# Kernel tuning notes

Hardware: AMD Instinct MI355X
Metric: run time of the kernel (lower is better)

Reference implementation:

```python
import jax, jax.numpy as jnp
import numpy as np

NUM_HEADS = 12

def setup_inputs() -> dict:
    key = jax.random.key(0)
    ks = jax.random.split(key, 8)
    B, N, C = 8, 1024, 768
    s = 1.0 / np.sqrt(C)
    return {
        "x": jax.random.normal(ks[0], (B, N, C), jnp.float32),
        "head_mask": jnp.ones((B, NUM_HEADS), jnp.float32),
        "q_w": jax.random.normal(ks[1], (C, C), jnp.float32) * s,
        "q_b": jnp.zeros((C,), jnp.float32),
        "k_w": jax.random.normal(ks[2], (C, C), jnp.float32) * s,
        "k_b": jnp.zeros((C,), jnp.float32),
        "v_w": jax.random.normal(ks[3], (C, C), jnp.float32) * s,
        "v_b": jnp.zeros((C,), jnp.float32),
        "proj_w": jax.random.normal(ks[4], (C, C), jnp.float32) * s,
        "proj_b": jnp.zeros((C,), jnp.float32),
    }

def reference(x, head_mask, q_w, q_b, k_w, k_b, v_w, v_b, proj_w, proj_b):
    B, N, C = x.shape
    H = NUM_HEADS
    d = C // H
    scale = d ** -0.5
    # torch Linear: y = x @ W.T + b; reshape to [B,H,N,d]
    q = (x @ q_w.T + q_b).reshape(B, N, H, d).transpose(0, 2, 1, 3)
    k = (x @ k_w.T + k_b).reshape(B, N, H, d).transpose(0, 2, 1, 3)
    v = (x @ v_w.T + v_b).reshape(B, N, H, d).transpose(0, 2, 1, 3)
    attn = jnp.einsum('bhnd,bhmd->bhnm', q, k) * scale
    attn = jax.nn.softmax(attn, axis=-1)
    y = jnp.einsum('bhnm,bhmd->bhnd', attn, v)
    # head_mask applied per head [B,H,1,1]
    y = y * head_mask[:, :, None, None]
    out = y.transpose(0, 2, 1, 3).reshape(B, N, C)
    # head_mask repeated per head_dim, applied to flattened channels [B,1,C]
    hm_flat = jnp.repeat(head_mask, d, axis=1)[:, None, :]
    out = out * hm_flat
    return out @ proj_w.T + proj_b
```

## Files before the change

kernel.cpp:

```cpp
#include <hip/hip_runtime.h>

typedef _Float16 half_t;
typedef _Float16 half2_t __attribute__((ext_vector_type(2)));
typedef _Float16 half4_t __attribute__((ext_vector_type(4)));
typedef _Float16 half8 __attribute__((ext_vector_type(8)));
typedef float f32x4 __attribute__((ext_vector_type(4)));
typedef float f32x16 __attribute__((ext_vector_type(16)));
typedef unsigned uint4v __attribute__((ext_vector_type(4)));

__device__ __forceinline__ void gload_lds16(const void* g, void* l) {
    __builtin_amdgcn_global_load_lds(
        (const __attribute__((address_space(1))) void*)g,
        (__attribute__((address_space(3))) void*)l, 16, 0, 0);
}

__global__ __launch_bounds__(256) void cast_f32_f16(const float* __restrict__ s,
                                                    half_t* __restrict__ d, int n) {
    const int stride = gridDim.x * blockDim.x;
    for (int i = blockIdx.x * blockDim.x + threadIdx.x; i * 4 < n; i += stride) {
        const float4 v = *(const float4*)(s + (long)i * 4);
        half4_t h = {(half_t)v.x, (half_t)v.y, (half_t)v.z, (half_t)v.w};
        *(half4_t*)(d + (long)i * 4) = h;
    }
}

__global__ __launch_bounds__(256) void cast_w4(const float* __restrict__ w0,
                                               const float* __restrict__ w1,
                                               const float* __restrict__ w2,
                                               const float* __restrict__ w3,
                                               half_t* __restrict__ d) {
    const int i = blockIdx.x * blockDim.x + threadIdx.x;
    const int which = i / 147456;
    const int off = i - which * 147456;
    const float* s = which == 0 ? w0 : which == 1 ? w1 : which == 2 ? w2 : w3;
    const float4 v = *(const float4*)(s + (long)off * 4);
    half4_t h = {(half_t)v.x, (half_t)v.y, (half_t)v.z, (half_t)v.w};
    *(half4_t*)(d + (long)i * 4) = h;
}

__global__ __launch_bounds__(256) void concat_bias(const float* __restrict__ a,
                                                   const float* __restrict__ b,
                                                   const float* __restrict__ c,
                                                   float* __restrict__ o) {
    int i = blockIdx.x * blockDim.x + threadIdx.x;
    if (i < 768) o[i] = a[i];
    else if (i < 1536) o[i] = b[i - 768];
    else if (i < 2304) o[i] = c[i - 1536];
}

__global__ __launch_bounds__(512) void gemm_qkv(const half_t* __restrict__ A,
                                                const half_t* __restrict__ W,
                                                const float* __restrict__ bias,
                                                half_t* __restrict__ qkv,
                                                half_t* __restrict__ Vt) {
    constexpr int Kdim = 768, Ndim = 2304, NT = Kdim / 64;
    alignas(16) __shared__ half_t Ah[2][256 * 64];
    alignas(16) __shared__ half_t Wh[2][192 * 64];

    const int t = threadIdx.x, l = t & 63, wv = t >> 6;
    const int wr = wv >> 2, wc = wv & 3;
    const int m0 = blockIdx.x * 256, n0 = blockIdx.y * 192;

    f32x4 acc[8][3] = {};

    const int srow_g = wv * 8 + (l >> 3);
    const int schunk = l & 7;

    const half_t* Ag = A + (long)m0 * Kdim;
    const half_t* Wg = W + (long)n0 * Kdim;

    auto STAGE = [&](int tile, int buf) {
        const int k0 = tile * 64;
#pragma unroll
        for (int ra = 0; ra < 4; ++ra) {
            const int row = ra * 64 + srow_g;
            const int sc_ = (schunk ^ (row & 7)) * 8;
            gload_lds16(Ag + (long)row * Kdim + k0 + sc_,
                        &Ah[buf][(ra * 64 + wv * 8) * 64]);
        }
#pragma unroll
        for (int rw = 0; rw < 3; ++rw) {
            const int row = rw * 64 + srow_g;
            const int sc_ = (schunk ^ (row & 7)) * 8;
            gload_lds16(Wg + (long)row * Kdim + k0 + sc_,
                        &Wh[buf][(rw * 64 + wv * 8) * 64]);
        }
    };

    STAGE(0, 0);
    STAGE(1, 1);

    for (int tt = 0; tt < NT; ++tt) {
        const int buf = tt & 1;
        if (tt < NT - 1) {
            asm volatile("s_waitcnt vmcnt(7)" ::: "memory");
        } else {
            asm volatile("s_waitcnt vmcnt(0)" ::: "memory");
        }
        __builtin_amdgcn_s_barrier();
        asm volatile("" ::: "memory");

#pragma unroll
        for (int ks = 0; ks < 2; ++ks) {
            const int kc = ks * 4 + (l >> 4);
            half8 bfr[3], afr[8];
#pragma unroll
            for (int nf = 0; nf < 3; ++nf) {
                const int row = wc * 48 + nf * 16 + (l & 15);
                bfr[nf] = *(const half8*)&Wh[buf][row * 64 + (kc ^ (row & 7)) * 8];
            }
#pragma unroll
            for (int mf = 0; mf < 8; ++mf) {
                const int row = wr * 128 + mf * 16 + (l & 15);
                afr[mf] = *(const half8*)&Ah[buf][row * 64 + (kc ^ (row & 7)) * 8];
            }
            __builtin_amdgcn_s_setprio(1);
#pragma unroll
            for (int mf = 0; mf < 8; ++mf)
#pragma unroll
                for (int nf = 0; nf < 3; ++nf)
                    acc[mf][nf] = __builtin_amdgcn_mfma_f32_16x16x32_f16(
                        afr[mf], bfr[nf], acc[mf][nf], 0, 0, 0);
            __builtin_amdgcn_s_setprio(0);
        }

        asm volatile("" ::: "memory");
        __builtin_amdgcn_s_barrier();
        if (tt + 2 < NT) STAGE(tt + 2, buf);
    }

    const bool vreg = (blockIdx.y >= 8);
#pragma unroll
    for (int nf = 0; nf < 3; ++nf) {
        const int col = n0 + wc * 48 + nf * 16 + (l & 15);
        const float bb = bias[col];
        if (!vreg) {
#pragma unroll
            for (int mf = 0; mf < 8; ++mf) {
                const int row = m0 + wr * 128 + mf * 16 + (l >> 4) * 4;
#pragma unroll
                for (int r = 0; r < 4; ++r)
                    qkv[(long)(row + r) * Ndim + col] = (half_t)(acc[mf][nf][r] + bb);
            }
        } else {
            const int hd = col - 1536;
            const int hidx = hd >> 6, d = hd & 63;
#pragma unroll
            for (int mf = 0; mf < 8; ++mf) {
                const int row = m0 + wr * 128 + mf * 16 + (l >> 4) * 4;
                const int b = row >> 10, n = row & 1023;
                half4_t pk;
#pragma unroll
                for (int r = 0; r < 4; ++r) pk[r] = (half_t)(acc[mf][nf][r] + bb);
                *(half4_t*)(Vt + ((long)((b * 12 + hidx) * 64 + d)) * 1024 + n) = pk;
            }
        }
    }
}

template <typename OutT>
__global__ __launch_bounds__(256) void gemm_bt(const half_t* __restrict__ A,
                                               const half_t* __restrict__ W,
                                               const float* __restrict__ bias,
                                               OutT* __restrict__ C,
                                               int M, int N, int K) {
    alignas(16) __shared__ half_t Ah[128 * 32];
    alignas(16) __shared__ half_t Wh[128 * 32];
    const int t = threadIdx.x;
    const int l = t & 63, w = t >> 6;
    const int m0 = blockIdx.x * 128, n0 = blockIdx.y * 128;
    const int wr = w >> 1, wc = w & 1;

    f32x4 acc[4][4] = {};

    const int srow = w * 16 + (l >> 2);
    const int scol = (l & 3) * 8;
    const half_t* Ag = A + (long)(m0 + srow) * K + scol;
    const half_t* Wg = W + (long)(n0 + srow) * K + scol;
    half_t* lA0 = &Ah[(w * 16) * 32];
    half_t* lA1 = &Ah[(w * 16 + 64) * 32];
    half_t* lW0 = &Wh[(w * 16) * 32];
    half_t* lW1 = &Wh[(w * 16 + 64) * 32];

    for (int k0 = 0; k0 < K; k0 += 32) {
        gload_lds16(Ag + k0, lA0);
        gload_lds16(Ag + (long)64 * K + k0, lA1);
        gload_lds16(Wg + k0, lW0);
        gload_lds16(Wg + (long)64 * K + k0, lW1);
        __syncthreads();

        half8 af[4], bf[4];
        const int ak = (l >> 4) * 8;
#pragma unroll
        for (int m = 0; m < 4; ++m)
            af[m] = *(const half8*)&Ah[(wr * 64 + m * 16 + (l & 15)) * 32 + ak];
#pragma unroll
        for (int n = 0; n < 4; ++n)
            bf[n] = *(const half8*)&Wh[(wc * 64 + n * 16 + (l & 15)) * 32 + ak];
#pragma unroll
        for (int m = 0; m < 4; ++m)
#pragma unroll
            for (int n = 0; n < 4; ++n)
                acc[m][n] = __builtin_amdgcn_mfma_f32_16x16x32_f16(af[m], bf[n], acc[m][n], 0, 0, 0);
        __syncthreads();
    }

#pragma unroll
    for (int m = 0; m < 4; ++m) {
        const int row = m0 + wr * 64 + m * 16 + (l >> 4) * 4;
#pragma unroll
        for (int n = 0; n < 4; ++n) {
            const int col = n0 + wc * 64 + n * 16 + (l & 15);
            const float bb = bias ? bias[col] : 0.f;
#pragma unroll
            for (int r = 0; r < 4; ++r) {
                float v = acc[m][n][r] + bb;
                C[(long)(row + r) * N + col] = (OutT)v;
            }
        }
    }
}

__global__ __launch_bounds__(256) void attn5_kernel(const half_t* __restrict__ qkv,
                                                    const half_t* __restrict__ Vt,
                                                    const float* __restrict__ head_mask,
                                                    half_t* __restrict__ Y) {
    alignas(16) __shared__ half_t Kl[2][64 * 64];
    alignas(16) __shared__ half_t Vl[2][64 * 64];

    const int t = threadIdx.x, l = t & 63, wv = t >> 6;
    const int h2 = l >> 5, q32 = l & 31;
    const int bh = blockIdx.x, b = bh / 12, hh = bh % 12;
    const int q0 = blockIdx.y * 128 + wv * 32;

    half8 qf[4];
    {
        const half_t SC = (half_t)(0.125f * 1.44269504f);
        const half_t* Qp = qkv + ((long)(b * 1024 + q0 + q32)) * 2304 + hh * 64 + h2 * 8;
#pragma unroll
        for (int kd = 0; kd < 4; ++kd) {
            half8 v = *(const half8*)(Qp + kd * 16);
#pragma unroll
            for (int j = 0; j < 8; ++j) v[j] = v[j] * SC;
            qf[kd] = v;
        }
    }

    const half8 ONES = {(half_t)1, (half_t)1, (half_t)1, (half_t)1,
                        (half_t)1, (half_t)1, (half_t)1, (half_t)1};

    const half_t* Kg = qkv + (long)b * 1024 * 2304 + 768 + hh * 64;
    const half_t* Vg = Vt + (long)bh * 64 * 1024;

    const int srow_lo = (l >> 3);
    const int schunk = l & 7;

    auto STAGE = [&](int tile, int bf) {
#pragma unroll
        for (int c = 0; c < 2; ++c) {
            const int row = c * 32 + wv * 8 + srow_lo;
            const int sc_ = (schunk ^ (row & 7)) * 8;
            gload_lds16(Kg + (long)(tile * 64 + row) * 2304 + sc_,
                        &Kl[bf][(c * 32 + wv * 8) * 64]);
            gload_lds16(Vg + (long)row * 1024 + tile * 64 + sc_,
                        &Vl[bf][(c * 32 + wv * 8) * 64]);
        }
    };

    f32x16 o0 = {}, o1 = {}, lacc = {};

    STAGE(0, 0);

    for (int tt = 0; tt < 16; ++tt) {
        const int bf = tt & 1;
        if (tt < 15) {
            STAGE(tt + 1, bf ^ 1);
            asm volatile("s_waitcnt vmcnt(4)" ::: "memory");
        } else {
            asm volatile("s_waitcnt vmcnt(0)" ::: "memory");
        }
        __builtin_amdgcn_s_barrier();
        asm volatile("" ::: "memory");

        f32x16 s0 = {}, s1 = {};
        __builtin_amdgcn_s_setprio(1);
#pragma unroll
        for (int kd = 0; kd < 4; ++kd) {
            const int ch = ((kd * 2 + h2) ^ (q32 & 7)) * 8;
            half8 k0 = *(const half8*)&Kl[bf][q32 * 64 + ch];
            half8 k1 = *(const half8*)&Kl[bf][(32 + q32) * 64 + ch];
            s0 = __builtin_amdgcn_mfma_f32_32x32x16_f16(k0, qf[kd], s0, 0, 0, 0);
            s1 = __builtin_amdgcn_mfma_f32_32x32x16_f16(k1, qf[kd], s1, 0, 0, 0);
        }
        __builtin_amdgcn_s_setprio(0);

#pragma unroll
        for (int kc = 0; kc < 4; ++kc) {
            const f32x16& ss = (kc >> 1) ? s1 : s0;
            const int rb = (kc & 1) * 8;
            unsigned pw[4];
#pragma unroll
            for (int k2 = 0; k2 < 4; ++k2) {
                const float a = __builtin_amdgcn_exp2f(ss[rb + 2 * k2]);
                const float c = __builtin_amdgcn_exp2f(ss[rb + 2 * k2 + 1]);
                pw[k2] = __builtin_bit_cast(unsigned, __builtin_amdgcn_cvt_pkrtz(a, c));
            }
            uint4v uu = {pw[0], pw[1], pw[2], pw[3]};
            const half8 pf = __builtin_bit_cast(half8, uu);

            const int g0 = 2 * kc;
            const int a0 = q32 * 64 + ((g0 ^ (q32 & 7)) * 8) + 4 * h2;
            const int a1 = q32 * 64 + (((g0 + 1) ^ (q32 & 7)) * 8) + 4 * h2;
            const int r2 = 32 + q32;
            const int b0 = r2 * 64 + ((g0 ^ (r2 & 7)) * 8) + 4 * h2;
            const int b1 = r2 * 64 + (((g0 + 1) ^ (r2 & 7)) * 8) + 4 * h2;
            half4_t va0 = *(const half4_t*)&Vl[bf][a0];
            half4_t va1 = *(const half4_t*)&Vl[bf][a1];
            half4_t vb0 = *(const half4_t*)&Vl[bf][b0];
            half4_t vb1 = *(const half4_t*)&Vl[bf][b1];
            half8 vf0 = {va0[0], va0[1], va0[2], va0[3], va1[0], va1[1], va1[2], va1[3]};
            half8 vf1 = {vb0[0], vb0[1], vb0[2], vb0[3], vb1[0], vb1[1], vb1[2], vb1[3]};

            __builtin_amdgcn_s_setprio(1);
            o0 = __builtin_amdgcn_mfma_f32_32x32x16_f16(vf0, pf, o0, 0, 0, 0);
            o1 = __builtin_amdgcn_mfma_f32_32x32x16_f16(vf1, pf, o1, 0, 0, 0);
            lacc = __builtin_amdgcn_mfma_f32_32x32x16_f16(ONES, pf, lacc, 0, 0, 0);
            __builtin_amdgcn_s_setprio(0);
        }

        asm volatile("" ::: "memory");
        __builtin_amdgcn_s_barrier();
    }

    const float hmv = head_mask[b * 12 + hh];
    const float sc = hmv * hmv / lacc[0];
    half_t* Yp = Y + ((long)(b * 1024 + q0 + q32)) * 768 + hh * 64;
#pragma unroll
    for (int db = 0; db < 2; ++db) {
        const f32x16 oo = db ? o1 : o0;
#pragma unroll
        for (int rq = 0; rq < 4; ++rq) {
            half4_t pk;
#pragma unroll
            for (int i = 0; i < 4; ++i) pk[i] = (half_t)(oo[rq * 4 + i] * sc);
            *(half4_t*)(Yp + db * 32 + rq * 8 + h2 * 4) = pk;
        }
    }
}

extern "C" void kernel_launch(void* const* d_in, const int* in_sizes, int n_in,
                              void* d_out, int out_size, void* d_ws, size_t ws_size,
                              hipStream_t stream) {
    const float* x   = (const float*)d_in[0];
    const float* hm  = (const float*)d_in[1];
    const float* q_w = (const float*)d_in[2];
    const float* q_b = (const float*)d_in[3];
    const float* k_w = (const float*)d_in[4];
    const float* k_b = (const float*)d_in[5];
    const float* v_w = (const float*)d_in[6];
    const float* v_b = (const float*)d_in[7];
    const float* p_w = (const float*)d_in[8];
    const float* p_b = (const float*)d_in[9];
    float* out = (float*)d_out;

    char* ws = (char*)d_ws;
    half_t* xh  = (half_t*)(ws);
    half_t* wc  = (half_t*)(ws + 12582912);
    half_t* pwh = (half_t*)(ws + 16121856);
    float*  bc  = (float*)(ws + 17301504);
    half_t* qkv = (half_t*)(ws + 17310720);
    half_t* y   = (half_t*)(ws + 55059456);
    half_t* Vt = (ws_size >= (size_t)67642368 + 12582912)
                     ? (half_t*)(ws + 67642368)
                     : (half_t*)d_out;

    cast_f32_f16<<<2048, 256, 0, stream>>>(x, xh, 8192 * 768);
    cast_w4<<<2304, 256, 0, stream>>>(q_w, k_w, v_w, p_w, wc);
    concat_bias<<<9, 256, 0, stream>>>(q_b, k_b, v_b, bc);

    gemm_qkv<<<dim3(32, 12), 512, 0, stream>>>(xh, wc, bc, qkv, Vt);
    attn5_kernel<<<dim3(96, 8), 256, 0, stream>>>(qkv, Vt, hm, y);
    gemm_bt<float><<<dim3(64, 6), 256, 0, stream>>>(y, pwh, p_b, out, 8192, 768, 768);
}
```

Baseline: 132.8 us.

## Unify QKV and projection GEMMs into a double-buffered 128x128 swizzled kernel

```diff
diff --git a/kernel.cpp b/kernel.cpp
--- a/kernel.cpp
+++ b/kernel.cpp
@@ -48,20 +48,22 @@
     else if (i < 2304) o[i] = c[i - 1536];
 }
 
-__global__ __launch_bounds__(512) void gemm_qkv(const half_t* __restrict__ A,
-                                                const half_t* __restrict__ W,
-                                                const float* __restrict__ bias,
-                                                half_t* __restrict__ qkv,
-                                                half_t* __restrict__ Vt) {
-    constexpr int Kdim = 768, Ndim = 2304, NT = Kdim / 64;
-    alignas(16) __shared__ half_t Ah[2][256 * 64];
-    alignas(16) __shared__ half_t Wh[2][192 * 64];
+template <typename OutT, bool VSPLIT>
+__global__ __launch_bounds__(256) void gemm128(const half_t* __restrict__ A,
+                                               const half_t* __restrict__ W,
+                                               const float* __restrict__ bias,
+                                               OutT* __restrict__ C,
+                                               half_t* __restrict__ Vt,
+                                               const int N) {
+    constexpr int Kdim = 768, NT = 12;
+    alignas(16) __shared__ half_t Ah[2][128 * 64];
+    alignas(16) __shared__ half_t Wh[2][128 * 64];
 
     const int t = threadIdx.x, l = t & 63, wv = t >> 6;
-    const int wr = wv >> 2, wc = wv & 3;
-    const int m0 = blockIdx.x * 256, n0 = blockIdx.y * 192;
-
-    f32x4 acc[8][3] = {};
+    const int wr = wv >> 1, wc = wv & 1;
+    const int m0 = blockIdx.x * 128, n0 = blockIdx.y * 128;
+
+    f32x4 acc[4][4] = {};
 
     const int srow_g = wv * 8 + (l >> 3);
     const int schunk = l & 7;
@@ -72,18 +74,13 @@
     auto STAGE = [&](int tile, int buf) {
         const int k0 = tile * 64;
 #pragma unroll
-        for (int ra = 0; ra < 4; ++ra) {
-            const int row = ra * 64 + srow_g;
+        for (int g = 0; g < 4; ++g) {
+            const int row = g * 32 + srow_g;
             const int sc_ = (schunk ^ (row & 7)) * 8;
             gload_lds16(Ag + (long)row * Kdim + k0 + sc_,
-                        &Ah[buf][(ra * 64 + wv * 8) * 64]);
-        }
-#pragma unroll
-        for (int rw = 0; rw < 3; ++rw) {
-            const int row = rw * 64 + srow_g;
-            const int sc_ = (schunk ^ (row & 7)) * 8;
+                        &Ah[buf][(g * 32 + wv * 8) * 64]);
             gload_lds16(Wg + (long)row * Kdim + k0 + sc_,
-                        &Wh[buf][(rw * 64 + wv * 8) * 64]);
+                        &Wh[buf][(g * 32 + wv * 8) * 64]);
         }
     };
 
@@ -93,7 +90,7 @@
     for (int tt = 0; tt < NT; ++tt) {
         const int buf = tt & 1;
         if (tt < NT - 1) {
-            asm volatile("s_waitcnt vmcnt(7)" ::: "memory");
+            asm volatile("s_waitcnt vmcnt(8)" ::: "memory");
         } else {
             asm volatile("s_waitcnt vmcnt(0)" ::: "memory");
         }
@@ -103,24 +100,21 @@
 #pragma unroll
         for (int ks = 0; ks < 2; ++ks) {
             const int kc = ks * 4 + (l >> 4);
-            half8 bfr[3], afr[8];
-#pragma unroll
-            for (int nf = 0; nf < 3; ++nf) {
-                const int row = wc * 48 + nf * 16 + (l & 15);
-                bfr[nf] = *(const half8*)&Wh[buf][row * 64 + (kc ^ (row & 7)) * 8];
-            }
-#pragma unroll
-            for (int mf = 0; mf < 8; ++mf) {
-                const int row = wr * 128 + mf * 16 + (l & 15);
-                afr[mf] = *(const half8*)&Ah[buf][row * 64 + (kc ^ (row & 7)) * 8];
+            half8 afr[4], bfr[4];
+#pragma unroll
+            for (int i = 0; i < 4; ++i) {
+                const int arow = wr * 64 + i * 16 + (l & 15);
+                afr[i] = *(const half8*)&Ah[buf][arow * 64 + (kc ^ (arow & 7)) * 8];
+                const int brow = wc * 64 + i * 16 + (l & 15);
+                bfr[i] = *(const half8*)&Wh[buf][brow * 64 + (kc ^ (brow & 7)) * 8];
             }
             __builtin_amdgcn_s_setprio(1);
 #pragma unroll
-            for (int mf = 0; mf < 8; ++mf)
-#pragma unroll
-                for (int nf = 0; nf < 3; ++nf)
-                    acc[mf][nf] = __builtin_amdgcn_mfma_f32_16x16x32_f16(
-                        afr[mf], bfr[nf], acc[mf][nf], 0, 0, 0);
+            for (int mi = 0; mi < 4; ++mi)
+#pragma unroll
+                for (int ni = 0; ni < 4; ++ni)
+                    acc[mi][ni] = __builtin_amdgcn_mfma_f32_16x16x32_f16(
+                        afr[mi], bfr[ni], acc[mi][ni], 0, 0, 0);
             __builtin_amdgcn_s_setprio(0);
         }
 
@@ -129,93 +123,30 @@
         if (tt + 2 < NT) STAGE(tt + 2, buf);
     }
 
-    const bool vreg = (blockIdx.y >= 8);
-#pragma unroll
-    for (int nf = 0; nf < 3; ++nf) {
-        const int col = n0 + wc * 48 + nf * 16 + (l & 15);
+    const bool vtile = VSPLIT && (blockIdx.y >= 12);
+#pragma unroll
+    for (int ni = 0; ni < 4; ++ni) {
+        const int col = n0 + wc * 64 + ni * 16 + (l & 15);
         const float bb = bias[col];
-        if (!vreg) {
-#pragma unroll
-            for (int mf = 0; mf < 8; ++mf) {
-                const int row = m0 + wr * 128 + mf * 16 + (l >> 4) * 4;
+        if (!vtile) {
+#pragma unroll
+            for (int mi = 0; mi < 4; ++mi) {
+                const int row = m0 + wr * 64 + mi * 16 + (l >> 4) * 4;
 #pragma unroll
                 for (int r = 0; r < 4; ++r)
-                    qkv[(long)(row + r) * Ndim + col] = (half_t)(acc[mf][nf][r] + bb);
+                    C[(long)(row + r) * N + col] = (OutT)(acc[mi][ni][r] + bb);
             }
         } else {
             const int hd = col - 1536;
             const int hidx = hd >> 6, d = hd & 63;
 #pragma unroll
-            for (int mf = 0; mf < 8; ++mf) {
-                const int row = m0 + wr * 128 + mf * 16 + (l >> 4) * 4;
+            for (int mi = 0; mi < 4; ++mi) {
+                const int row = m0 + wr * 64 + mi * 16 + (l >> 4) * 4;
                 const int b = row >> 10, n = row & 1023;
                 half4_t pk;
 #pragma unroll
-                for (int r = 0; r < 4; ++r) pk[r] = (half_t)(acc[mf][nf][r] + bb);
+                for (int r = 0; r < 4; ++r) pk[r] = (half_t)(acc[mi][ni][r] + bb);
                 *(half4_t*)(Vt + ((long)((b * 12 + hidx) * 64 + d)) * 1024 + n) = pk;
-            }
-        }
-    }
-}
-
-template <typename OutT>
-__global__ __launch_bounds__(256) void gemm_bt(const half_t* __restrict__ A,
-                                               const half_t* __restrict__ W,
-                                               const float* __restrict__ bias,
-                                               OutT* __restrict__ C,
-                                               int M, int N, int K) {
-    alignas(16) __shared__ half_t Ah[128 * 32];
-    alignas(16) __shared__ half_t Wh[128 * 32];
-    const int t = threadIdx.x;
-    const int l = t & 63, w = t >> 6;
-    const int m0 = blockIdx.x * 128, n0 = blockIdx.y * 128;
-    const int wr = w >> 1, wc = w & 1;
-
-    f32x4 acc[4][4] = {};
-
-    const int srow = w * 16 + (l >> 2);
-    const int scol = (l & 3) * 8;
-    const half_t* Ag = A + (long)(m0 + srow) * K + scol;
-    const half_t* Wg = W + (long)(n0 + srow) * K + scol;
-    half_t* lA0 = &Ah[(w * 16) * 32];
-    half_t* lA1 = &Ah[(w * 16 + 64) * 32];
-    half_t* lW0 = &Wh[(w * 16) * 32];
-    half_t* lW1 = &Wh[(w * 16 + 64) * 32];
-
-    for (int k0 = 0; k0 < K; k0 += 32) {
-        gload_lds16(Ag + k0, lA0);
-        gload_lds16(Ag + (long)64 * K + k0, lA1);
-        gload_lds16(Wg + k0, lW0);
-        gload_lds16(Wg + (long)64 * K + k0, lW1);
-        __syncthreads();
-
-        half8 af[4], bf[4];
-        const int ak = (l >> 4) * 8;
-#pragma unroll
-        for (int m = 0; m < 4; ++m)
-            af[m] = *(const half8*)&Ah[(wr * 64 + m * 16 + (l & 15)) * 32 + ak];
-#pragma unroll
-        for (int n = 0; n < 4; ++n)
-            bf[n] = *(const half8*)&Wh[(wc * 64 + n * 16 + (l & 15)) * 32 + ak];
-#pragma unroll
-        for (int m = 0; m < 4; ++m)
-#pragma unroll
-            for (int n = 0; n < 4; ++n)
-                acc[m][n] = __builtin_amdgcn_mfma_f32_16x16x32_f16(af[m], bf[n], acc[m][n], 0, 0, 0);
-        __syncthreads();
-    }
-
-#pragma unroll
-    for (int m = 0; m < 4; ++m) {
-        const int row = m0 + wr * 64 + m * 16 + (l >> 4) * 4;
-#pragma unroll
-        for (int n = 0; n < 4; ++n) {
-            const int col = n0 + wc * 64 + n * 16 + (l & 15);
-            const float bb = bias ? bias[col] : 0.f;
-#pragma unroll
-            for (int r = 0; r < 4; ++r) {
-                float v = acc[m][n][r] + bb;
-                C[(long)(row + r) * N + col] = (OutT)v;
             }
         }
     }
@@ -378,7 +309,7 @@
     cast_w4<<<2304, 256, 0, stream>>>(q_w, k_w, v_w, p_w, wc);
     concat_bias<<<9, 256, 0, stream>>>(q_b, k_b, v_b, bc);
 
-    gemm_qkv<<<dim3(32, 12), 512, 0, stream>>>(xh, wc, bc, qkv, Vt);
+    gemm128<half_t, true><<<dim3(64, 18), 256, 0, stream>>>(xh, wc, bc, qkv, Vt, 2304);
     attn5_kernel<<<dim3(96, 8), 256, 0, stream>>>(qkv, Vt, hm, y);
-    gemm_bt<float><<<dim3(64, 6), 256, 0, stream>>>(y, pwh, p_b, out, 8192, 768, 768);
-}
+    gemm128<float, false><<<dim3(64, 6), 256, 0, stream>>>(y, pwh, p_b, out, nullptr, 768);
+}
```

New measurement: 114.7 us. -13.6%, faster.
